# Performance work log

Measured on AMD Instinct MI355X. Metric: run time of the kernel, lower is better.

The kernel has to match this reference:

```python
import jax, jax.numpy as jnp
import numpy as np

N, E, D, L, G = 50000, 625000, 128, 3, 64
EPS = 1e-5


def setup_inputs() -> dict:
    key = jax.random.key(0)
    ks = jax.random.split(key, 16)
    s = 1.0 / np.sqrt(D)
    inp = {
        "x": jax.random.normal(ks[0], (N, D), jnp.float32),
        "edge_index": jax.random.randint(ks[1], (2, E), 0, N, jnp.int64),
        "batch": jnp.sort(jax.random.randint(ks[2], (N,), 0, G, jnp.int64)),
        # node_emb
        "Wemb": jax.random.normal(ks[3], (D, D), jnp.float32) * s,
        "bemb": jnp.zeros((D,), jnp.float32),
        # per-layer params stacked on axis 0
        "Wscore": jax.random.normal(ks[4], (L, 1, D), jnp.float32) * s,
        "bscore": jnp.zeros((L, 1), jnp.float32),
        "Wfwd": jax.random.normal(ks[5], (L, D, D), jnp.float32) * s,
        "Wbwd": jax.random.normal(ks[6], (L, D, D), jnp.float32) * s,
        "Wself": jax.random.normal(ks[7], (L, D, D), jnp.float32) * s,
        "bself": jnp.zeros((L, D), jnp.float32),
        "Wcomb": jax.random.normal(ks[8], (L, D, 3 * D), jnp.float32) * s,
        "bcomb": jnp.zeros((L, D), jnp.float32),
        "gamma": jnp.ones((L, D), jnp.float32),
        "beta": jnp.zeros((L, D), jnp.float32),
    }
    return inp


def reference(x, edge_index, batch, Wemb, bemb, Wscore, bscore, Wfwd, Wbwd,
              Wself, bself, Wcomb, bcomb, gamma, beta):
    n = x.shape[0]
    src, dst = edge_index[0], edge_index[1]  # j (source), i (target)
    h = jax.nn.relu(x @ Wemb.T + bemb)       # dropout is eval-mode no-op
    for l in range(Wscore.shape[0]):
        identity = h
        scores = h @ Wscore[l].T + bscore[l]           # [N, 1]
        h_fwd = h @ Wfwd[l].T                          # [N, D]
        h_bwd = h @ Wbwd[l].T
        h_self = h @ Wself[l].T + bself[l]
        alpha = jax.nn.sigmoid(scores[src] - scores[dst])  # [E, 1]
        aggr_fwd = jax.ops.segment_sum(h_fwd[src] * alpha, dst, num_segments=n)
        aggr_bwd = jax.ops.segment_sum(h_bwd[src] * (1.0 - alpha), dst, num_segments=n)
        z = jnp.concatenate([h_self, aggr_fwd, aggr_bwd], axis=-1) @ Wcomb[l].T + bcomb[l]
        mu = jnp.mean(z, axis=-1, keepdims=True)
        var = jnp.var(z, axis=-1, keepdims=True)
        z = (z - mu) * jax.lax.rsqrt(var + EPS) * gamma[l] + beta[l]
        h = jax.nn.relu(z) + identity
    # global mean pool over graphs
    sums = jax.ops.segment_sum(h, batch, num_segments=G)
    cnt = jax.ops.segment_sum(jnp.ones((n,), h.dtype), batch, num_segments=G)
    return sums / jnp.maximum(cnt, 1.0)[:, None]
```

## Files before the change

kernel.cpp:

```cpp
#include <hip/hip_runtime.h>
#include <math.h>

#define EPS 1e-5f
#define PS 8
#define SW(row) (((row) & 7) << 4)

typedef __attribute__((ext_vector_type(8))) short short8;
typedef __attribute__((ext_vector_type(4))) float f32x4;

__device__ __forceinline__ float bf2f(unsigned short u) {
  union { unsigned i; float f; } c; c.i = ((unsigned)u) << 16; return c.f;
}
__device__ __forceinline__ float bflo(unsigned u) {
  union { unsigned i; float f; } c; c.i = u << 16; return c.f;
}
__device__ __forceinline__ float bfhi(unsigned u) {
  union { unsigned i; float f; } c; c.i = u & 0xFFFF0000u; return c.f;
}
__device__ __forceinline__ unsigned short f2bf(float f) {
  union { float f; unsigned i; } c; c.f = f;
  unsigned r = c.i + 0x7FFF + ((c.i >> 16) & 1);
  return (unsigned short)(r >> 16);
}

template <bool SCORE>
__global__ __launch_bounds__(256, 2) void embed_gemm(
    const ushort* __restrict__ A,
    const ushort* __restrict__ W,
    const float* __restrict__ bias,
    const float* __restrict__ Wsc, const float* __restrict__ bsc,
    ushort* __restrict__ hb, float* __restrict__ scores, int M) {
  __shared__ __align__(16) ushort As[64 * 128];
  __shared__ __align__(16) ushort Ws[128 * 128];
  __shared__ float lds3[64][2];

  const int t = threadIdx.x;
  const int lane = t & 63;
  const int w = t >> 6;
  const int wm = w >> 1, wn = w & 1;
  const int m0 = blockIdx.x * 64;
  const int l15 = lane & 15, l16 = lane >> 4;

  short8 ar[4], wr_[8];
#pragma unroll
  for (int it = 0; it < 4; ++it) {
    int chunk = it * 256 + t;
    int row = chunk >> 4;
    int b16 = chunk & 15;
    int grow = m0 + row; if (grow >= M) grow = M - 1;
    ar[it] = *(const short8*)(A + (size_t)grow * 128 + b16 * 8);
  }
#pragma unroll
  for (int it = 0; it < 8; ++it) {
    int chunk = it * 256 + t;
    int row = chunk >> 4;
    int b16 = chunk & 15;
    wr_[it] = *(const short8*)(W + (size_t)row * 128 + b16 * 8);
  }
#pragma unroll
  for (int it = 0; it < 4; ++it) {
    int chunk = it * 256 + t;
    int row = chunk >> 4, b = (chunk & 15) * 16;
    *(short8*)((char*)As + row * 256 + (b ^ SW(row))) = ar[it];
  }
#pragma unroll
  for (int it = 0; it < 8; ++it) {
    int chunk = it * 256 + t;
    int row = chunk >> 4, b = (chunk & 15) * 16;
    *(short8*)((char*)Ws + row * 256 + (b ^ SW(row))) = wr_[it];
  }
  __syncthreads();

  f32x4 acc[2][4];
#pragma unroll
  for (int i = 0; i < 2; ++i)
#pragma unroll
    for (int j = 0; j < 4; ++j) acc[i][j] = (f32x4){0.f, 0.f, 0.f, 0.f};

#pragma unroll
  for (int kk = 0; kk < 4; ++kk) {
    int cb = kk * 64 + l16 * 16;
    short8 a[2], b[4];
#pragma unroll
    for (int i = 0; i < 2; ++i) {
      int row = wm * 32 + i * 16 + l15;
      a[i] = *(const short8*)((const char*)As + row * 256 + (cb ^ SW(row)));
    }
#pragma unroll
    for (int j = 0; j < 4; ++j) {
      int row = wn * 64 + j * 16 + l15;
      b[j] = *(const short8*)((const char*)Ws + row * 256 + (cb ^ SW(row)));
    }
#pragma unroll
    for (int i = 0; i < 2; ++i)
#pragma unroll
      for (int j = 0; j < 4; ++j)
        acc[i][j] = __builtin_amdgcn_mfma_f32_16x16x32_bf16(a[i], b[j], acc[i][j], 0, 0, 0);
  }

#pragma unroll
  for (int i = 0; i < 2; ++i)
#pragma unroll
    for (int r = 0; r < 4; ++r) {
      int row = m0 + wm * 32 + i * 16 + l16 * 4 + r;
      bool valid = row < M;
      float psc = 0.f;
#pragma unroll
      for (int j = 0; j < 4; ++j) {
        int colw = wn * 64 + j * 16 + l15;
        float v = acc[i][j][r] + bias[colw];
        v = fmaxf(v, 0.f);
        if (valid) hb[(size_t)row * 128 + colw] = f2bf(v);
        if (SCORE) psc += v * Wsc[colw];
      }
      if (SCORE) {
#pragma unroll
        for (int mm = 1; mm <= 8; mm <<= 1) psc += __shfl_xor(psc, mm, 64);
        if (l15 == 0) lds3[wm * 32 + i * 16 + l16 * 4 + r][wn] = psc;
      }
    }
  if (SCORE) {
    __syncthreads();
    if (wn == 0 && l15 == 0) {
#pragma unroll
      for (int i = 0; i < 2; ++i)
#pragma unroll
        for (int r = 0; r < 4; ++r) {
          int rl = wm * 32 + i * 16 + l16 * 4 + r;
          int row = blockIdx.x * 64 + rl;
          if (row < M) scores[row] = lds3[rl][0] + lds3[rl][1] + bsc[0];
        }
    }
  }
}

template <bool SCORE>
__global__ __launch_bounds__(256, 2) void layer_gemm(
    const ushort* __restrict__ A0,
    const ushort* __restrict__ A1,
    const ushort* __restrict__ W,
    const float* __restrict__ bias,
    const float* __restrict__ gamma, const float* __restrict__ beta,
    const float* __restrict__ Wsc, const float* __restrict__ bsc,
    ushort* __restrict__ hb, float* __restrict__ scores, int M) {
  __shared__ __align__(16) ushort As[64 * 192];
  __shared__ __align__(16) ushort Ws[128 * 192];
  __shared__ float lds1[64][2];
  __shared__ float lds2[64][2];
  __shared__ float lds3[64][2];

  const int t = threadIdx.x;
  const int lane = t & 63;
  const int w = t >> 6;
  const int wm = w >> 1, wn = w & 1;
  const int m0 = blockIdx.x * 64;
  const int l15 = lane & 15, l16 = lane >> 4;

  f32x4 acc[2][4];
#pragma unroll
  for (int i = 0; i < 2; ++i)
#pragma unroll
    for (int j = 0; j < 4; ++j) acc[i][j] = (f32x4){0.f, 0.f, 0.f, 0.f};

#pragma unroll
  for (int hf = 0; hf < 2; ++hf) {
    short8 ar[6], wr_[12];
#pragma unroll
    for (int it = 0; it < 6; ++it) {
      int chunk = it * 256 + t;
      int row = chunk / 24;
      int b16 = chunk % 24;
      int ec = hf * 192 + b16 * 8;
      int grow = m0 + row; if (grow >= M) grow = M - 1;
      const ushort* src = (ec < 128) ? (A0 + (size_t)grow * 128 + ec)
                                     : (A1 + (size_t)grow * 256 + (ec - 128));
      ar[it] = *(const short8*)src;
    }
#pragma unroll
    for (int it = 0; it < 12; ++it) {
      int chunk = it * 256 + t;
      int row = chunk / 24;
      int b16 = chunk % 24;
      wr_[it] = *(const short8*)(W + (size_t)row * 384 + hf * 192 + b16 * 8);
    }
    __syncthreads();
#pragma unroll
    for (int it = 0; it < 6; ++it) {
      int chunk = it * 256 + t;
      int row = chunk / 24, b = (chunk % 24) * 16;
      *(short8*)((char*)As + row * 384 + (b ^ SW(row))) = ar[it];
    }
#pragma unroll
    for (int it = 0; it < 12; ++it) {
      int chunk = it * 256 + t;
      int row = chunk / 24, b = (chunk % 24) * 16;
      *(short8*)((char*)Ws + row * 384 + (b ^ SW(row))) = wr_[it];
    }
    __syncthreads();
#pragma unroll
    for (int kk = 0; kk < 6; ++kk) {
      int cb = kk * 64 + l16 * 16;
      short8 a[2], b[4];
#pragma unroll
      for (int i = 0; i < 2; ++i) {
        int row = wm * 32 + i * 16 + l15;
        a[i] = *(const short8*)((const char*)As + row * 384 + (cb ^ SW(row)));
      }
#pragma unroll
      for (int j = 0; j < 4; ++j) {
        int row = wn * 64 + j * 16 + l15;
        b[j] = *(const short8*)((const char*)Ws + row * 384 + (cb ^ SW(row)));
      }
#pragma unroll
      for (int i = 0; i < 2; ++i)
#pragma unroll
        for (int j = 0; j < 4; ++j)
          acc[i][j] = __builtin_amdgcn_mfma_f32_16x16x32_bf16(a[i], b[j], acc[i][j], 0, 0, 0);
    }
  }

#pragma unroll
  for (int i = 0; i < 2; ++i)
#pragma unroll
    for (int r = 0; r < 4; ++r) {
      float p1 = 0.f, p2 = 0.f;
#pragma unroll
      for (int j = 0; j < 4; ++j) {
        int colw = wn * 64 + j * 16 + l15;
        float v = acc[i][j][r] + bias[colw];
        acc[i][j][r] = v;
        p1 += v;
        p2 += v * v;
      }
#pragma unroll
      for (int mm = 1; mm <= 8; mm <<= 1) {
        p1 += __shfl_xor(p1, mm, 64);
        p2 += __shfl_xor(p2, mm, 64);
      }
      if (l15 == 0) {
        int rl = wm * 32 + i * 16 + l16 * 4 + r;
        lds1[rl][wn] = p1;
        lds2[rl][wn] = p2;
      }
    }
  __syncthreads();
#pragma unroll
  for (int i = 0; i < 2; ++i)
#pragma unroll
    for (int r = 0; r < 4; ++r) {
      int rl = wm * 32 + i * 16 + l16 * 4 + r;
      int row = m0 + rl;
      bool valid = row < M;
      float s1 = lds1[rl][0] + lds1[rl][1];
      float s2 = lds2[rl][0] + lds2[rl][1];
      float mu = s1 * (1.f / 128.f);
      float var = s2 * (1.f / 128.f) - mu * mu;
      float rs = rsqrtf(var + EPS);
      float psc = 0.f;
#pragma unroll
      for (int j = 0; j < 4; ++j) {
        int colw = wn * 64 + j * 16 + l15;
        float v = acc[i][j][r];
        float o = (v - mu) * rs * gamma[colw] + beta[colw];
        o = fmaxf(o, 0.f);
        float res = o;
        if (valid) {
          res = o + bf2f(hb[(size_t)row * 128 + colw]);
          hb[(size_t)row * 128 + colw] = f2bf(res);
        }
        if (SCORE) psc += res * Wsc[colw];
      }
      if (SCORE) {
#pragma unroll
        for (int mm = 1; mm <= 8; mm <<= 1) psc += __shfl_xor(psc, mm, 64);
        if (l15 == 0) lds3[rl][wn] = psc;
      }
    }
  if (SCORE) {
    __syncthreads();
    if (wn == 0 && l15 == 0) {
#pragma unroll
      for (int i = 0; i < 2; ++i)
#pragma unroll
        for (int r = 0; r < 4; ++r) {
          int rl = wm * 32 + i * 16 + l16 * 4 + r;
          int row = m0 + rl;
          if (row < M) scores[row] = lds3[rl][0] + lds3[rl][1] + bsc[0];
        }
    }
  }
}

__global__ __launch_bounds__(256) void wpre_kernel(
    const float* __restrict__ Wcomb, const float* __restrict__ Wself,
    const float* __restrict__ Wfwd, const float* __restrict__ Wbwd,
    ushort* __restrict__ Wbig) {
  const int l = blockIdx.x / 3, p = blockIdx.x % 3;
  const float* Wc = Wcomb + (size_t)l * 128 * 384;
  const float* Wp = (p == 0 ? Wself : (p == 1 ? Wfwd : Wbwd)) + (size_t)l * 128 * 128;
  __shared__ float Bs[128][132];
  const int t = threadIdx.x;
  for (int i = t; i < 16384; i += 256) Bs[i >> 7][i & 127] = Wp[i];
  __syncthreads();
  const int r = t >> 1;
  const int c0 = (t & 1) * 64;
  float acc[64];
#pragma unroll
  for (int c = 0; c < 64; ++c) acc[c] = 0.f;
  for (int k = 0; k < 128; ++k) {
    float a = Wc[(size_t)r * 384 + p * 128 + k];
#pragma unroll
    for (int c4 = 0; c4 < 16; ++c4) {
      float4 b4 = *(const float4*)&Bs[k][c0 + c4 * 4];
      acc[c4 * 4 + 0] = fmaf(a, b4.x, acc[c4 * 4 + 0]);
      acc[c4 * 4 + 1] = fmaf(a, b4.y, acc[c4 * 4 + 1]);
      acc[c4 * 4 + 2] = fmaf(a, b4.z, acc[c4 * 4 + 2]);
      acc[c4 * 4 + 3] = fmaf(a, b4.w, acc[c4 * 4 + 3]);
    }
  }
  ushort* o = Wbig + (size_t)l * 128 * 384 + (size_t)r * 384 + p * 128 + c0;
#pragma unroll
  for (int c = 0; c < 64; ++c) o[c] = f2bf(acc[c]);
}

__global__ void bpre_kernel(const float* __restrict__ Wcomb, const float* __restrict__ bself,
                            const float* __restrict__ bcomb, float* __restrict__ biasc, int L) {
  int idx = blockIdx.x * 128 + threadIdx.x;
  if (idx >= L * 128) return;
  int l = idx >> 7;
  const float* Wc = Wcomb + (size_t)l * 128 * 384 + (size_t)(idx & 127) * 384;
  const float* bs = bself + (size_t)l * 128;
  float acc = bcomb[idx];
  for (int k = 0; k < 128; ++k) acc = fmaf(Wc[k], bs[k], acc);
  biasc[idx] = acc;
}

__global__ void f2b_kernel(const float* __restrict__ in, ushort* __restrict__ out, int n4) {
  int i = blockIdx.x * 256 + threadIdx.x;
  if (i < n4) {
    float4 v = ((const float4*)in)[i];
    ushort4 o;
    o.x = f2bf(v.x); o.y = f2bf(v.y); o.z = f2bf(v.z); o.w = f2bf(v.w);
    ((ushort4*)out)[i] = o;
  }
}

__global__ void hist_kernel(const int* __restrict__ dst, int* __restrict__ counts, int E) {
  int e = blockIdx.x * 256 + threadIdx.x;
  if (e < E) atomicAdd(&counts[dst[e]], 1);
}

__global__ __launch_bounds__(256) void scan1_kernel(
    const int* __restrict__ c, int* __restrict__ ex, int* __restrict__ partials, int n) {
  __shared__ int sd[256];
  int t = threadIdx.x, b = blockIdx.x;
  int base = b * 1024 + t * 4;
  int v0 = (base + 0 < n) ? c[base + 0] : 0;
  int v1 = (base + 1 < n) ? c[base + 1] : 0;
  int v2 = (base + 2 < n) ? c[base + 2] : 0;
  int v3 = (base + 3 < n) ? c[base + 3] : 0;
  int tot = v0 + v1 + v2 + v3;
  sd[t] = tot;
  __syncthreads();
  for (int off = 1; off < 256; off <<= 1) {
    int x = (t >= off) ? sd[t - off] : 0;
    __syncthreads();
    sd[t] += x;
    __syncthreads();
  }
  int p = sd[t] - tot;
  if (base + 0 < n) ex[base + 0] = p;
  if (base + 1 < n) ex[base + 1] = p + v0;
  if (base + 2 < n) ex[base + 2] = p + v0 + v1;
  if (base + 3 < n) ex[base + 3] = p + v0 + v1 + v2;
  if (t == 255) partials[b] = sd[255];
}

__global__ __launch_bounds__(256) void scan2_kernel(int* __restrict__ partials, int nb) {
  __shared__ int sd[256];
  int t = threadIdx.x;
  int v = (t < nb) ? partials[t] : 0;
  sd[t] = v;
  __syncthreads();
  for (int off = 1; off < 256; off <<= 1) {
    int x = (t >= off) ? sd[t - off] : 0;
    __syncthreads();
    sd[t] += x;
    __syncthreads();
  }
  if (t < nb) partials[t] = sd[t] - v;
}

__global__ void scan3_kernel(const int* __restrict__ ex, const int* __restrict__ partials,
                             int* __restrict__ indptr, int n, int E) {
  int i = blockIdx.x * 256 + threadIdx.x;
  if (i < n) indptr[i] = ex[i] + partials[i >> 10];
  if (i == 0) indptr[n] = E;
}

__global__ void scatter_kernel(const int* __restrict__ ei, int* __restrict__ cursor,
                               int* __restrict__ ssrc, int E) {
  int e = blockIdx.x * 256 + threadIdx.x;
  if (e >= E) return;
  int s = ei[e];
  int d = ei[E + e];
  int pos = atomicAdd(&cursor[d], 1);
  ssrc[pos] = s;
}

__global__ __launch_bounds__(256) void aggr_kernel(
    const int* __restrict__ indptr, const int* __restrict__ ssrc,
    const float* __restrict__ scores, const ushort* __restrict__ hb,
    ushort* __restrict__ uv, int Nn) {
  int node = blockIdx.x * 4 + (threadIdx.x >> 6);
  if (node >= Nn) return;
  int lane = threadIdx.x & 63;
  int beg = indptr[node], end = indptr[node + 1];
  float si = scores[node];
  float u0 = 0.f, u1 = 0.f, t0 = 0.f, t1 = 0.f;
  for (int ebase = beg; ebase < end; ebase += 64) {
    int cnt = min(64, end - ebase);
    int sv = 0;
    float al = 0.f;
    if (lane < cnt) {
      sv = ssrc[ebase + lane];
      al = 1.f / (1.f + __expf(si - scores[sv]));
    }
    for (int e = 0; e < cnt; ++e) {
      int s_e = __shfl(sv, e, 64);
      float a_e = __shfl(al, e, 64);
      unsigned vv = *(const unsigned*)(hb + (size_t)s_e * 128 + lane * 2);
      float f0 = bflo(vv), f1 = bfhi(vv);
      u0 = fmaf(a_e, f0, u0);
      u1 = fmaf(a_e, f1, u1);
      t0 += f0;
      t1 += f1;
    }
  }
  unsigned pu = (unsigned)f2bf(u0) | ((unsigned)f2bf(u1) << 16);
  unsigned pv = (unsigned)f2bf(t0 - u0) | ((unsigned)f2bf(t1 - u1) << 16);
  *(unsigned*)(uv + (size_t)node * 256 + lane * 2) = pu;
  *(unsigned*)(uv + (size_t)node * 256 + 128 + lane * 2) = pv;
}

__global__ __launch_bounds__(128) void pool_stage_kernel(
    const ushort* __restrict__ hb, const int* __restrict__ batch,
    float* __restrict__ partial, int M) {
  int g = blockIdx.x, s = blockIdx.y, d = threadIdx.x;
  int lo = 0, hi = M;
  while (lo < hi) { int mid = (lo + hi) >> 1; if (batch[mid] < g) lo = mid + 1; else hi = mid; }
  int b0 = lo;
  hi = M;
  while (lo < hi) { int mid = (lo + hi) >> 1; if (batch[mid] <= g) lo = mid + 1; else hi = mid; }
  int b1 = lo;
  int len = b1 - b0;
  int chunk = (len + PS - 1) / PS;
  int r0 = b0 + s * chunk;
  int r1 = min(b1, r0 + chunk);
  float acc = 0.f;
  for (int i = r0; i < r1; ++i) acc += bf2f(hb[(size_t)i * 128 + d]);
  partial[((size_t)g * PS + s) * 128 + d] = acc;
}

__global__ void pool_final_kernel(const float* __restrict__ partial,
                                  const int* __restrict__ batch,
                                  float* __restrict__ out, int M, int G) {
  int idx = blockIdx.x * 256 + threadIdx.x;
  if (idx >= G * 128) return;
  int g = idx >> 7, d = idx & 127;
  float acc = 0.f;
#pragma unroll
  for (int s = 0; s < PS; ++s) acc += partial[((size_t)g * PS + s) * 128 + d];
  int lo = 0, hi = M;
  while (lo < hi) { int mid = (lo + hi) >> 1; if (batch[mid] < g) lo = mid + 1; else hi = mid; }
  int b0 = lo;
  hi = M;
  while (lo < hi) { int mid = (lo + hi) >> 1; if (batch[mid] <= g) lo = mid + 1; else hi = mid; }
  int c = lo - b0;
  out[idx] = acc / (float)(c > 0 ? c : 1);
}

extern "C" void kernel_launch(void* const* d_in, const int* in_sizes, int n_in,
                              void* d_out, int out_size, void* d_ws, size_t ws_size,
                              hipStream_t stream) {
  const float* x      = (const float*)d_in[0];
  const int*   ei     = (const int*)d_in[1];
  const int*   batch  = (const int*)d_in[2];
  const float* Wemb   = (const float*)d_in[3];
  const float* bemb   = (const float*)d_in[4];
  const float* Wscore = (const float*)d_in[5];
  const float* bscore = (const float*)d_in[6];
  const float* Wfwd   = (const float*)d_in[7];
  const float* Wbwd   = (const float*)d_in[8];
  const float* Wself  = (const float*)d_in[9];
  const float* bself  = (const float*)d_in[10];
  const float* Wcomb  = (const float*)d_in[11];
  const float* bcomb  = (const float*)d_in[12];
  const float* gamma  = (const float*)d_in[13];
  const float* beta   = (const float*)d_in[14];

  const int N = in_sizes[0] / 128;
  const int E = in_sizes[1] / 2;
  const int L = in_sizes[5] / 128;
  const int G = out_size / 128;
  float* out = (float*)d_out;

  char* p = (char*)d_ws;
  auto alloc = [&](size_t bytes) -> char* {
    char* r = p;
    p += (bytes + 255) & ~(size_t)255;
    return r;
  };
  ushort* xb     = (ushort*)alloc((size_t)N * 128 * 2);
  ushort* hb16   = (ushort*)alloc((size_t)N * 128 * 2);
  ushort* uv     = (ushort*)alloc((size_t)N * 256 * 2);
  float*  scores = (float*)alloc((size_t)N * 4);
  ushort* Wemb_b = (ushort*)alloc(16384 * 2);
  ushort* Wbig   = (ushort*)alloc((size_t)L * 128 * 384 * 2);
  float*  biasc  = (float*)alloc((size_t)L * 128 * 4);
  int* counts    = (int*)alloc((size_t)N * 4);
  int* ex        = (int*)alloc((size_t)N * 4);
  int* partials  = (int*)alloc(1024);
  int* indptr    = (int*)alloc((size_t)(N + 1) * 4);
  int* cursor    = (int*)alloc((size_t)N * 4);
  int* ssrc      = (int*)alloc((size_t)E * 4);
  float* pool_p  = (float*)alloc((size_t)G * PS * 128 * 4);

  const int gb = (N + 63) / 64;

  f2b_kernel<<<(N * 32 + 255) / 256, 256, 0, stream>>>(x, xb, N * 32);
  f2b_kernel<<<16, 256, 0, stream>>>(Wemb, Wemb_b, 4096);
  wpre_kernel<<<3 * L, 256, 0, stream>>>(Wcomb, Wself, Wfwd, Wbwd, Wbig);
  bpre_kernel<<<L, 128, 0, stream>>>(Wcomb, bself, bcomb, biasc, L);

  hipMemsetAsync(counts, 0, (size_t)N * 4, stream);
  hist_kernel<<<(E + 255) / 256, 256, 0, stream>>>(ei + E, counts, E);
  int nb = (N + 1023) / 1024;
  scan1_kernel<<<nb, 256, 0, stream>>>(counts, ex, partials, N);
  scan2_kernel<<<1, 256, 0, stream>>>(partials, nb);
  scan3_kernel<<<(N + 255) / 256, 256, 0, stream>>>(ex, partials, indptr, N, E);
  hipMemcpyAsync(cursor, indptr, (size_t)N * 4, hipMemcpyDeviceToDevice, stream);
  scatter_kernel<<<(E + 255) / 256, 256, 0, stream>>>(ei, cursor, ssrc, E);

  embed_gemm<true><<<gb, 256, 0, stream>>>(xb, Wemb_b, bemb, Wscore, bscore,
                                           hb16, scores, N);

  for (int l = 0; l < L; ++l) {
    aggr_kernel<<<(N + 3) / 4, 256, 0, stream>>>(indptr, ssrc, scores, hb16, uv, N);
    if (l < L - 1) {
      layer_gemm<true><<<gb, 256, 0, stream>>>(
          hb16, uv, Wbig + (size_t)l * 128 * 384, biasc + (size_t)l * 128,
          gamma + (size_t)l * 128, beta + (size_t)l * 128,
          Wscore + (size_t)(l + 1) * 128, bscore + (l + 1), hb16, scores, N);
    } else {
      layer_gemm<false><<<gb, 256, 0, stream>>>(
          hb16, uv, Wbig + (size_t)l * 128 * 384, biasc + (size_t)l * 128,
          gamma + (size_t)l * 128, beta + (size_t)l * 128,
          nullptr, nullptr, hb16, scores, N);
    }
  }

  pool_stage_kernel<<<dim3(G, PS), 128, 0, stream>>>(hb16, batch, pool_p, N);
  pool_final_kernel<<<(G * 128 + 255) / 256, 256, 0, stream>>>(pool_p, batch, out, N, G);
}
```

Baseline: 495.2 us.

## Fuse x fp32-to-bf16 conversion into embed GEMM and unroll aggregation gather loop

The embedding GEMM now reads fp32 x directly and converts it to bf16 in registers. This removes the separate conversion kernel and its round trip through a bf16 workspace buffer. Separately, the edge aggregation loop is unrolled by four so four neighbour-row gathers are in flight at once, exposing more memory-level parallelism. The GEMM loads twice as many bytes for A per tile, and the unrolled loop needs a few more registers.

Result: faster. 433.0 us (-12.6%).

```diff
diff --git a/kernel.cpp b/kernel.cpp
--- a/kernel.cpp
+++ b/kernel.cpp
@@ -25,7 +25,7 @@
 
 template <bool SCORE>
 __global__ __launch_bounds__(256, 2) void embed_gemm(
-    const ushort* __restrict__ A,
+    const float* __restrict__ X,
     const ushort* __restrict__ W,
     const float* __restrict__ bias,
     const float* __restrict__ Wsc, const float* __restrict__ bsc,
@@ -48,7 +48,15 @@
     int row = chunk >> 4;
     int b16 = chunk & 15;
     int grow = m0 + row; if (grow >= M) grow = M - 1;
-    ar[it] = *(const short8*)(A + (size_t)grow * 128 + b16 * 8);
+    const float* xr = X + (size_t)grow * 128 + b16 * 8;
+    float4 f0 = *(const float4*)xr;
+    float4 f1 = *(const float4*)(xr + 4);
+    short8 v;
+    v[0] = (short)f2bf(f0.x); v[1] = (short)f2bf(f0.y);
+    v[2] = (short)f2bf(f0.z); v[3] = (short)f2bf(f0.w);
+    v[4] = (short)f2bf(f1.x); v[5] = (short)f2bf(f1.y);
+    v[6] = (short)f2bf(f1.z); v[7] = (short)f2bf(f1.w);
+    ar[it] = v;
   }
 #pragma unroll
   for (int it = 0; it < 8; ++it) {
@@ -426,15 +434,33 @@
       sv = ssrc[ebase + lane];
       al = 1.f / (1.f + __expf(si - scores[sv]));
     }
-    for (int e = 0; e < cnt; ++e) {
+    int e = 0;
+    for (; e + 4 <= cnt; e += 4) {
+      int s0 = __shfl(sv, e, 64),     s1 = __shfl(sv, e + 1, 64);
+      int s2 = __shfl(sv, e + 2, 64), s3 = __shfl(sv, e + 3, 64);
+      float a0 = __shfl(al, e, 64),     a1 = __shfl(al, e + 1, 64);
+      float a2 = __shfl(al, e + 2, 64), a3 = __shfl(al, e + 3, 64);
+      unsigned v0 = *(const unsigned*)(hb + (size_t)s0 * 128 + lane * 2);
+      unsigned v1 = *(const unsigned*)(hb + (size_t)s1 * 128 + lane * 2);
+      unsigned v2 = *(const unsigned*)(hb + (size_t)s2 * 128 + lane * 2);
+      unsigned v3 = *(const unsigned*)(hb + (size_t)s3 * 128 + lane * 2);
+      float f;
+      f = bflo(v0); u0 = fmaf(a0, f, u0); t0 += f;
+      f = bfhi(v0); u1 = fmaf(a0, f, u1); t1 += f;
+      f = bflo(v1); u0 = fmaf(a1, f, u0); t0 += f;
+      f = bfhi(v1); u1 = fmaf(a1, f, u1); t1 += f;
+      f = bflo(v2); u0 = fmaf(a2, f, u0); t0 += f;
+      f = bfhi(v2); u1 = fmaf(a2, f, u1); t1 += f;
+      f = bflo(v3); u0 = fmaf(a3, f, u0); t0 += f;
+      f = bfhi(v3); u1 = fmaf(a3, f, u1); t1 += f;
+    }
+    for (; e < cnt; ++e) {
       int s_e = __shfl(sv, e, 64);
       float a_e = __shfl(al, e, 64);
       unsigned vv = *(const unsigned*)(hb + (size_t)s_e * 128 + lane * 2);
       float f0 = bflo(vv), f1 = bfhi(vv);
-      u0 = fmaf(a_e, f0, u0);
-      u1 = fmaf(a_e, f1, u1);
-      t0 += f0;
-      t1 += f1;
+      u0 = fmaf(a_e, f0, u0); t0 += f0;
+      u1 = fmaf(a_e, f1, u1); t1 += f1;
     }
   }
   unsigned pu = (unsigned)f2bf(u0) | ((unsigned)f2bf(u1) << 16);
@@ -511,7 +537,6 @@
     p += (bytes + 255) & ~(size_t)255;
     return r;
   };
-  ushort* xb     = (ushort*)alloc((size_t)N * 128 * 2);
   ushort* hb16   = (ushort*)alloc((size_t)N * 128 * 2);
   ushort* uv     = (ushort*)alloc((size_t)N * 256 * 2);
   float*  scores = (float*)alloc((size_t)N * 4);
@@ -528,7 +553,6 @@
 
   const int gb = (N + 63) / 64;
 
-  f2b_kernel<<<(N * 32 + 255) / 256, 256, 0, stream>>>(x, xb, N * 32);
   f2b_kernel<<<16, 256, 0, stream>>>(Wemb, Wemb_b, 4096);
   wpre_kernel<<<3 * L, 256, 0, stream>>>(Wcomb, Wself, Wfwd, Wbwd, Wbig);
   bpre_kernel<<<L, 128, 0, stream>>>(Wcomb, bself, bcomb, biasc, L);
@@ -542,7 +566,7 @@
   hipMemcpyAsync(cursor, indptr, (size_t)N * 4, hipMemcpyDeviceToDevice, stream);
   scatter_kernel<<<(E + 255) / 256, 256, 0, stream>>>(ei, cursor, ssrc, E);
 
-  embed_gemm<true><<<gb, 256, 0, stream>>>(xb, Wemb_b, bemb, Wscore, bscore,
+  embed_gemm<true><<<gb, 256, 0, stream>>>(x, Wemb_b, bemb, Wscore, bscore,
                                            hb16, scores, N);
 
   for (int l = 0; l < L; ++l) {
```
